# Optimization experiments

Measured on AMD Instinct MI355X. Metric: run time of the kernel, lower is better.

The kernel has to match this reference:

```python
import jax, jax.numpy as jnp
import numpy as np

N = 10000
E = 160000
D = 512
EDGE_DIM = 128
L = 3
LN_EPS = 1e-5


def setup_inputs() -> dict:
    key = jax.random.key(0)
    ks = jax.random.split(key, 16)
    s = 0.02
    return {
        "x": jax.random.normal(ks[0], (N, D), dtype=jnp.float32),
        "edge_index": jax.random.randint(ks[1], (2, E), 0, N, dtype=jnp.int64),
        "edge_attr": jax.random.normal(ks[2], (E, EDGE_DIM), dtype=jnp.float32),
        # per-layer GINEConv edge projection Linear(edge_dim -> d_in); here d_in == D for all layers
        "We": jax.random.normal(ks[3], (L, EDGE_DIM, D), dtype=jnp.float32) * s,
        "be": jnp.zeros((L, D), dtype=jnp.float32),
        "eps": jnp.zeros((L,), dtype=jnp.float32),  # train_eps=True, init 0
        # per-layer MLP: Linear(D->D), ReLU, Linear(D->D)
        "W1": jax.random.normal(ks[4], (L, D, D), dtype=jnp.float32) * s,
        "b1": jnp.zeros((L, D), dtype=jnp.float32),
        "W2": jax.random.normal(ks[5], (L, D, D), dtype=jnp.float32) * s,
        "b2": jnp.zeros((L, D), dtype=jnp.float32),
        # per-layer LayerNorm
        "gamma": jnp.ones((L, D), dtype=jnp.float32),
        "beta": jnp.zeros((L, D), dtype=jnp.float32),
        # final Linear(D->D)
        "Wf": jax.random.normal(ks[6], (D, D), dtype=jnp.float32) * s,
        "bf": jnp.zeros((D,), dtype=jnp.float32),
    }


def reference(x, edge_index, edge_attr, We, be, eps, W1, b1, W2, b2, gamma, beta, Wf, bf):
    src = edge_index[0]  # x_j (source)
    dst = edge_index[1]  # aggregation target i
    n = x.shape[0]
    h = x
    for l in range(L):
        # GINEConv message: relu(x_j + lin(edge_attr)), scatter-add at dst
        e = jax.nn.relu(h[src] + edge_attr @ We[l] + be[l])  # [E, D]
        agg = jax.ops.segment_sum(e, dst, num_segments=n)     # [N, D]
        g = (1.0 + eps[l]) * h + agg
        # 2-layer MLP
        g = jax.nn.relu(g @ W1[l] + b1[l]) @ W2[l] + b2[l]
        # ReLU then LayerNorm (dropout p=0)
        g = jax.nn.relu(g)
        mu = jnp.mean(g, axis=-1, keepdims=True)
        var = jnp.mean(jnp.square(g - mu), axis=-1, keepdims=True)
        h = (g - mu) * jax.lax.rsqrt(var + LN_EPS) * gamma[l] + beta[l]
    return h @ Wf + bf
```

## Files before the change

### kernel.cpp

```cpp
#include <hip/hip_runtime.h>

#define NN 10000
#define EE 160000
#define DD 512
#define EDIM 128
#define LLAYERS 3
#define LN_EPS 1e-5f

typedef __attribute__((ext_vector_type(8))) short bf16x8;
typedef __attribute__((ext_vector_type(4))) float f32x4;

__device__ __forceinline__ unsigned short f2b(float f) {
    union { float f; unsigned u; } v; v.f = f;
    unsigned r = (v.u + 0x7fffu + ((v.u >> 16) & 1u)) >> 16;
    return (unsigned short)r;
}
__device__ __forceinline__ float b2f(unsigned short s) {
    union { unsigned u; float f; } v; v.u = ((unsigned)s) << 16;
    return v.f;
}
__device__ __forceinline__ unsigned short f2h(float f) {
    _Float16 h = (_Float16)f;
    unsigned short u; __builtin_memcpy(&u, &h, 2);
    return u;
}
__device__ __forceinline__ float h2f(unsigned short u) {
    _Float16 h; __builtin_memcpy(&h, &u, 2);
    return (float)h;
}

__global__ __launch_bounds__(256) void hist_kernel(
    const int* __restrict__ dstv, int* __restrict__ deg)
{
    int e = blockIdx.x * 256 + threadIdx.x;
    if (e < EE) atomicAdd(&deg[dstv[e]], 1);
}

__global__ __launch_bounds__(256) void scan_kernel(
    const int* __restrict__ deg, int* __restrict__ base, int* __restrict__ cursor)
{
    __shared__ int sums[256];
    const int t = threadIdx.x;
    const int CH = 40;
    int lo = t * CH;
    int hi = lo + CH; if (hi > NN) hi = NN;
    int s = 0;
    for (int i = lo; i < hi; i++) s += deg[i];
    sums[t] = s;
    __syncthreads();
    for (int off = 1; off < 256; off <<= 1) {
        int v = (t >= off) ? sums[t - off] : 0;
        __syncthreads();
        sums[t] += v;
        __syncthreads();
    }
    int run = (t == 0) ? 0 : sums[t - 1];
    for (int i = lo; i < hi; i++) {
        base[i] = run; cursor[i] = run;
        run += deg[i];
    }
}

__global__ __launch_bounds__(256) void scatter_kernel(
    const int* __restrict__ srcv, const int* __restrict__ dstv,
    int* __restrict__ cursor,
    int* __restrict__ ssrc, int* __restrict__ sdst, int* __restrict__ perm)
{
    int e = blockIdx.x * 256 + threadIdx.x;
    if (e < EE) {
        int d = dstv[e];
        int pos = atomicAdd(&cursor[d], 1);
        ssrc[pos] = srcv[e];
        sdst[pos] = d;
        perm[pos] = e;
    }
}

__global__ __launch_bounds__(256) void transpose_bf16_kernel(
    const float* __restrict__ src, unsigned short* __restrict__ dst, int K, int N)
{
    __shared__ float t[32][33];
    const int x = threadIdx.x & 31;
    const int y = threadIdx.x >> 5;
    const int bn = blockIdx.x * 32;
    const int bk = blockIdx.y * 32;
    #pragma unroll
    for (int j = 0; j < 32; j += 8)
        t[y + j][x] = src[(size_t)(bk + y + j) * N + bn + x];
    __syncthreads();
    #pragma unroll
    for (int j = 0; j < 32; j += 8)
        dst[(size_t)(bn + y + j) * K + bk + x] = f2b(t[x][y + j]);
}

__global__ __launch_bounds__(256) void cvt_bf16_kernel(
    const float* __restrict__ src, unsigned short* __restrict__ dst)
{
    int i = blockIdx.x * 256 + threadIdx.x;
    float4 v = ((const float4*)src)[i];
    uint2 o;
    o.x = (unsigned)f2b(v.x) | ((unsigned)f2b(v.y) << 16);
    o.y = (unsigned)f2b(v.z) | ((unsigned)f2b(v.w) << 16);
    ((uint2*)dst)[i] = o;
}

__global__ __launch_bounds__(256) void gather_cvt_kernel(
    const float* __restrict__ ea, const int* __restrict__ perm,
    unsigned short* __restrict__ out, int elo)
{
    int i = blockIdx.x * 256 + threadIdx.x;
    int r = i >> 5, c4 = (i & 31) * 4;
    const float* p = ea + (size_t)perm[elo + r] * EDIM + c4;
    float4 v = *(const float4*)p;
    uint2 o;
    o.x = (unsigned)f2b(v.x) | ((unsigned)f2b(v.y) << 16);
    o.y = (unsigned)f2b(v.z) | ((unsigned)f2b(v.w) << 16);
    *(uint2*)&out[(size_t)r * EDIM + c4] = o;
}

#define MEP 136
__global__ __launch_bounds__(256) void msg_gemm(
    const unsigned short* __restrict__ Abf,
    const unsigned short* __restrict__ WeT,
    const float* __restrict__ be,
    unsigned short* __restrict__ msg)
{
    __shared__ unsigned short sA[128 * MEP];

    const int tid  = threadIdx.x;
    const int c0   = blockIdx.x * 128;
    const int e0   = blockIdx.y * 128;
    const int w    = tid >> 6;
    const int lane = tid & 63;
    const int quad = lane >> 4;
    const int l16  = lane & 15;
    const int mh   = (w & 1) * 64;
    const int nsl  = (w >> 1) * 64;

    for (int i = tid; i < 128 * 16; i += 256) {
        int r = i >> 4, seg = i & 15;
        *(uint4*)&sA[r * MEP + seg * 8] =
            *(const uint4*)&Abf[(size_t)(e0 + r) * EDIM + seg * 8];
    }
    __syncthreads();

    f32x4 acc[4][4];
    #pragma unroll
    for (int mr = 0; mr < 4; mr++)
        #pragma unroll
        for (int nb = 0; nb < 4; nb++)
            acc[mr][nb] = (f32x4){0.f, 0.f, 0.f, 0.f};

    #pragma unroll
    for (int ks = 0; ks < 4; ks++) {
        const int ko = ks * 32 + quad * 8;
        bf16x8 a[4];
        #pragma unroll
        for (int mr = 0; mr < 4; mr++)
            a[mr] = *(const bf16x8*)&sA[(mh + mr * 16 + l16) * MEP + ko];
        bf16x8 b[4];
        #pragma unroll
        for (int nb = 0; nb < 4; nb++)
            b[nb] = *(const bf16x8*)&WeT[(size_t)(c0 + nsl + nb * 16 + l16) * EDIM + ko];
        #pragma unroll
        for (int mr = 0; mr < 4; mr++)
            #pragma unroll
            for (int nb = 0; nb < 4; nb++)
                acc[mr][nb] = __builtin_amdgcn_mfma_f32_16x16x32_bf16(a[mr], b[nb], acc[mr][nb], 0, 0, 0);
    }

    #pragma unroll
    for (int mr = 0; mr < 4; mr++) {
        const int rb = e0 + mh + mr * 16 + quad * 4;
        #pragma unroll
        for (int nb = 0; nb < 4; nb++) {
            const int c = c0 + nsl + nb * 16 + l16;
            const float bv = be[c];
            const f32x4 v = acc[mr][nb];
            #pragma unroll
            for (int reg = 0; reg < 4; reg++)
                msg[(size_t)(rb + reg) * DD + c] = f2h(v[reg] + bv);
        }
    }
}

__global__ __launch_bounds__(256) void agg_kernel(
    const unsigned short* __restrict__ h_bf,
    const unsigned short* __restrict__ msg,
    const int* __restrict__ ssrc,
    const int* __restrict__ basep,
    const int* __restrict__ degp,
    const float* __restrict__ epsp,
    float* __restrict__ aggp,
    unsigned short* __restrict__ aprime,
    int elo, int ehi, int first, int last)
{
    const int d  = blockIdx.x;
    const int b0 = basep[d];
    const int b1 = b0 + degp[d];
    int lo = b0 > elo ? b0 : elo;
    int hi = b1 < ehi ? b1 : ehi;
    if (!first && !last && lo >= hi) return;

    const int t  = threadIdx.x;
    const int c2 = t * 2;

    float a0 = 0.f, a1 = 0.f;
    if (!first) {
        float2 pv = *(const float2*)&aggp[(size_t)d * DD + c2];
        a0 = pv.x; a1 = pv.y;
    }
    for (int p = lo; p < hi; p++) {
        const int s = ssrc[p];
        unsigned mv = *(const unsigned*)&msg[(size_t)(p - elo) * DD + c2];
        unsigned hv = *(const unsigned*)&h_bf[(size_t)s * DD + c2];
        a0 += fmaxf(h2f((unsigned short)(mv & 0xffffu)) + b2f((unsigned short)(hv & 0xffffu)), 0.f);
        a1 += fmaxf(h2f((unsigned short)(mv >> 16))     + b2f((unsigned short)(hv >> 16)),     0.f);
    }
    if (last) {
        const float es = 1.0f + epsp[0];
        unsigned hv = *(const unsigned*)&h_bf[(size_t)d * DD + c2];
        unsigned o = (unsigned)f2b(es * b2f((unsigned short)(hv & 0xffffu)) + a0)
                   | ((unsigned)f2b(es * b2f((unsigned short)(hv >> 16))    + a1) << 16);
        *(unsigned*)&aprime[(size_t)d * DD + c2] = o;
    } else {
        *(float2*)&aggp[(size_t)d * DD + c2] = make_float2(a0, a1);
    }
}

#define GPITCH 136
template <bool RELU, bool OUTBF>
__global__ __launch_bounds__(256) void mfma_gemm(
    const unsigned short* __restrict__ A,
    const unsigned short* __restrict__ WT,
    const float* __restrict__ bias,
    void* __restrict__ Cout, int M)
{
    __shared__ unsigned short sA[64 * GPITCH];
    __shared__ unsigned short sB[128 * GPITCH];

    const int tid  = threadIdx.x;
    const int m0   = blockIdx.x * 64;
    const int c0   = blockIdx.y * 128;
    const int w    = tid >> 6;
    const int lane = tid & 63;
    const int quad = lane >> 4;
    const int l16  = lane & 15;
    const int mh   = (w & 1) * 32;
    const int nsl  = (w >> 1) * 64;

    f32x4 acc[2][4];
    #pragma unroll
    for (int mr = 0; mr < 2; mr++)
        #pragma unroll
        for (int nb = 0; nb < 4; nb++)
            acc[mr][nb] = (f32x4){0.f, 0.f, 0.f, 0.f};

    for (int kc = 0; kc < DD; kc += 128) {
        __syncthreads();
        for (int i = tid; i < 64 * 16; i += 256) {
            int r = i >> 4, seg = i & 15;
            int gm = m0 + r;
            uint4 v = make_uint4(0u, 0u, 0u, 0u);
            if (gm < M)
                v = *(const uint4*)&A[(size_t)gm * DD + kc + seg * 8];
            *(uint4*)&sA[r * GPITCH + seg * 8] = v;
        }
        for (int i = tid; i < 128 * 16; i += 256) {
            int r = i >> 4, seg = i & 15;
            *(uint4*)&sB[r * GPITCH + seg * 8] =
                *(const uint4*)&WT[(size_t)(c0 + r) * DD + kc + seg * 8];
        }
        __syncthreads();
        #pragma unroll
        for (int ks = 0; ks < 4; ks++) {
            const int ko = ks * 32 + quad * 8;
            bf16x8 a0 = *(const bf16x8*)&sA[(mh + l16) * GPITCH + ko];
            bf16x8 a1 = *(const bf16x8*)&sA[(mh + 16 + l16) * GPITCH + ko];
            bf16x8 b[4];
            #pragma unroll
            for (int nb = 0; nb < 4; nb++)
                b[nb] = *(const bf16x8*)&sB[(nsl + nb * 16 + l16) * GPITCH + ko];
            #pragma unroll
            for (int nb = 0; nb < 4; nb++) {
                acc[0][nb] = __builtin_amdgcn_mfma_f32_16x16x32_bf16(a0, b[nb], acc[0][nb], 0, 0, 0);
                acc[1][nb] = __builtin_amdgcn_mfma_f32_16x16x32_bf16(a1, b[nb], acc[1][nb], 0, 0, 0);
            }
        }
    }

    #pragma unroll
    for (int mr = 0; mr < 2; mr++) {
        const int rbase = m0 + mh + mr * 16 + quad * 4;
        #pragma unroll
        for (int nb = 0; nb < 4; nb++) {
            const int c = c0 + nsl + nb * 16 + l16;
            const float bv = bias[c];
            const f32x4 v = acc[mr][nb];
            #pragma unroll
            for (int reg = 0; reg < 4; reg++) {
                int gm = rbase + reg;
                if (gm < M) {
                    float val = v[reg] + bv;
                    if (RELU) val = fmaxf(val, 0.f);
                    if (OUTBF) ((unsigned short*)Cout)[(size_t)gm * DD + c] = f2b(val);
                    else       ((float*)Cout)[(size_t)gm * DD + c] = val;
                }
            }
        }
    }
}

__global__ __launch_bounds__(256) void relu_ln_kernel(
    const unsigned short* __restrict__ g2,
    const float* __restrict__ gamma,
    const float* __restrict__ beta,
    unsigned short* __restrict__ hout)
{
    __shared__ float ss[4], ssq[4];
    const int row = blockIdx.x;
    const int tid = threadIdx.x;
    const unsigned short* gr = g2 + (size_t)row * DD;

    float v0 = fmaxf(b2f(gr[tid]), 0.f);
    float v1 = fmaxf(b2f(gr[tid + 256]), 0.f);
    float s  = v0 + v1;
    float sq = v0 * v0 + v1 * v1;
    #pragma unroll
    for (int off = 32; off > 0; off >>= 1) {
        s  += __shfl_down(s, off);
        sq += __shfl_down(sq, off);
    }
    const int wave = tid >> 6;
    const int lane = tid & 63;
    if (lane == 0) { ss[wave] = s; ssq[wave] = sq; }
    __syncthreads();
    if (tid == 0) {
        float S  = ss[0] + ss[1] + ss[2] + ss[3];
        float SQ = ssq[0] + ssq[1] + ssq[2] + ssq[3];
        float mu = S * (1.f / 512.f);
        float var = SQ * (1.f / 512.f) - mu * mu;
        ss[0]  = mu;
        ssq[0] = rsqrtf(var + LN_EPS);
    }
    __syncthreads();
    float mu = ss[0], rstd = ssq[0];
    hout[(size_t)row * DD + tid] =
        f2b((v0 - mu) * rstd * gamma[tid] + beta[tid]);
    hout[(size_t)row * DD + tid + 256] =
        f2b((v1 - mu) * rstd * gamma[tid + 256] + beta[tid + 256]);
}

extern "C" void kernel_launch(void* const* d_in, const int* in_sizes, int n_in,
                              void* d_out, int out_size, void* d_ws, size_t ws_size,
                              hipStream_t stream)
{
    (void)in_sizes; (void)n_in; (void)out_size;

    const float* x          = (const float*)d_in[0];
    const int*   edge_index = (const int*)d_in[1];
    const float* edge_attr  = (const float*)d_in[2];
    const float* We         = (const float*)d_in[3];
    const float* be         = (const float*)d_in[4];
    const float* eps        = (const float*)d_in[5];
    const float* W1         = (const float*)d_in[6];
    const float* b1         = (const float*)d_in[7];
    const float* W2         = (const float*)d_in[8];
    const float* b2         = (const float*)d_in[9];
    const float* gamma      = (const float*)d_in[10];
    const float* beta       = (const float*)d_in[11];
    const float* Wf         = (const float*)d_in[12];
    const float* bf         = (const float*)d_in[13];

    unsigned short* h_bf   = (unsigned short*)d_ws;
    unsigned short* aprime = h_bf + (size_t)NN * DD;
    unsigned short* t1     = aprime + (size_t)NN * DD;
    unsigned short* t2     = t1 + (size_t)NN * DD;
    unsigned short* WeT    = t2 + (size_t)NN * DD;
    unsigned short* W1T    = WeT + (size_t)LLAYERS * DD * EDIM;
    unsigned short* W2T    = W1T + (size_t)LLAYERS * DD * DD;
    unsigned short* WfT    = W2T + (size_t)LLAYERS * DD * DD;
    int* deg    = (int*)(WfT + (size_t)DD * DD);
    int* basep  = deg + NN;
    int* cursor = basep + NN;
    int* ssrc   = cursor + NN;
    int* sdst   = ssrc + EE;
    int* perm   = sdst + EE;
    float* aggp = (float*)(perm + EE);
    unsigned short* ea_hf = (unsigned short*)(aggp + (size_t)NN * DD);

    size_t used = (size_t)((unsigned char*)ea_hf - (unsigned char*)d_ws);
    size_t rem  = ws_size > used ? ws_size - used : 0;
    const size_t EA_FULL  = (size_t)EE * EDIM * 2;
    const size_t MSG_FULL = (size_t)EE * DD * 2;
    int ea_full; long long capE;
    if (rem >= EA_FULL + MSG_FULL) {
        ea_full = 1; capE = EE;
    } else if (rem >= EA_FULL + (size_t)32 * 1024 * 1024) {
        ea_full = 1;
        capE = (long long)((rem - EA_FULL) / ((size_t)DD * 2)) & ~127LL;
    } else {
        ea_full = 0;
        capE = (long long)(rem / ((size_t)(EDIM + DD) * 2)) & ~127LL;
        if (capE < 128) capE = 128;
    }
    if (capE > EE) capE = EE;
    unsigned short* msg = ea_hf + (ea_full ? (size_t)EE * EDIM : (size_t)capE * EDIM);

    const int* srcv = edge_index;
    const int* dstv = edge_index + EE;

    hipMemsetAsync(deg, 0, NN * sizeof(int), stream);
    hist_kernel<<<dim3((EE + 255) / 256), 256, 0, stream>>>(dstv, deg);
    scan_kernel<<<dim3(1), 256, 0, stream>>>(deg, basep, cursor);
    scatter_kernel<<<dim3((EE + 255) / 256), 256, 0, stream>>>(
        srcv, dstv, cursor, ssrc, sdst, perm);

    cvt_bf16_kernel<<<dim3(NN * DD / 4 / 256), 256, 0, stream>>>(x, h_bf);
    for (int l = 0; l < LLAYERS; l++) {
        transpose_bf16_kernel<<<dim3(DD / 32, EDIM / 32), 256, 0, stream>>>(
            We + (size_t)l * EDIM * DD, WeT + (size_t)l * DD * EDIM, EDIM, DD);
        transpose_bf16_kernel<<<dim3(DD / 32, DD / 32), 256, 0, stream>>>(
            W1 + (size_t)l * DD * DD, W1T + (size_t)l * DD * DD, DD, DD);
        transpose_bf16_kernel<<<dim3(DD / 32, DD / 32), 256, 0, stream>>>(
            W2 + (size_t)l * DD * DD, W2T + (size_t)l * DD * DD, DD, DD);
    }
    transpose_bf16_kernel<<<dim3(DD / 32, DD / 32), 256, 0, stream>>>(Wf, WfT, DD, DD);

    if (ea_full)
        gather_cvt_kernel<<<dim3(EE / 8), 256, 0, stream>>>(edge_attr, perm, ea_hf, 0);

    dim3 ggrid((NN + 63) / 64, DD / 128);

    const int nch = (int)((EE + capE - 1) / capE);
    for (int l = 0; l < LLAYERS; l++) {
        for (int c = 0; c < nch; c++) {
            const int elo = (int)((long long)c * capE);
            const int cnt = (EE - elo < capE) ? (EE - elo) : (int)capE;
            if (!ea_full)
                gather_cvt_kernel<<<dim3(cnt / 8), 256, 0, stream>>>(edge_attr, perm, ea_hf, elo);
            const unsigned short* Ab = ea_full ? ea_hf + (size_t)elo * EDIM : ea_hf;
            msg_gemm<<<dim3(4, cnt / 128), 256, 0, stream>>>(
                Ab, WeT + (size_t)l * DD * EDIM, be + (size_t)l * DD, msg);
            agg_kernel<<<dim3(NN), 256, 0, stream>>>(
                h_bf, msg, ssrc, basep, deg, eps + l, aggp, aprime,
                elo, elo + cnt, c == 0 ? 1 : 0, c == nch - 1 ? 1 : 0);
        }
        mfma_gemm<true, true><<<ggrid, 256, 0, stream>>>(
            aprime, W1T + (size_t)l * DD * DD, b1 + (size_t)l * DD, t1, NN);
        mfma_gemm<false, true><<<ggrid, 256, 0, stream>>>(
            t1, W2T + (size_t)l * DD * DD, b2 + (size_t)l * DD, t2, NN);
        relu_ln_kernel<<<dim3(NN), 256, 0, stream>>>(
            t2, gamma + (size_t)l * DD, beta + (size_t)l * DD, h_bf);
    }
    mfma_gemm<false, false><<<ggrid, 256, 0, stream>>>(h_bf, WfT, bf, d_out, NN);
}
```

Before: 834.6 us.

## Unify GEMMs into 128x128 tile kernel with LDS-staged coalesced stores, unroll aggregation

Replaces the separate message GEMM and the 64x128 MLP GEMM with one templated 128x128-tile kernel. It reads B fragments straight from global memory instead of staging them in LDS, and writes 16-bit outputs through LDS so the global stores are coalesced and wide. Message stores are nontemporal. The aggregation loop is unrolled by four and its message reads use nontemporal loads, so more independent loads are in flight. This raises per-block work and register use, gives fewer blocks for the N-sized GEMMs, and makes B reads uncached in LDS.

```diff
diff --git a/kernel.cpp b/kernel.cpp
--- a/kernel.cpp
+++ b/kernel.cpp
@@ -9,6 +9,7 @@
 
 typedef __attribute__((ext_vector_type(8))) short bf16x8;
 typedef __attribute__((ext_vector_type(4))) float f32x4;
+typedef __attribute__((ext_vector_type(4))) unsigned int u32x4;
 
 __device__ __forceinline__ unsigned short f2b(float f) {
     union { float f; unsigned u; } v; v.f = f;
@@ -119,17 +120,18 @@
 }
 
 #define MEP 136
-__global__ __launch_bounds__(256) void msg_gemm(
-    const unsigned short* __restrict__ Abf,
-    const unsigned short* __restrict__ WeT,
-    const float* __restrict__ be,
-    unsigned short* __restrict__ msg)
+template <int KDIM, bool RELU, int OUT>
+__global__ __launch_bounds__(256) void tile_gemm(
+    const unsigned short* __restrict__ A,
+    const unsigned short* __restrict__ WT,
+    const float* __restrict__ bias,
+    void* __restrict__ Cout, int M)
 {
     __shared__ unsigned short sA[128 * MEP];
 
     const int tid  = threadIdx.x;
     const int c0   = blockIdx.x * 128;
-    const int e0   = blockIdx.y * 128;
+    const int m0   = blockIdx.y * 128;
     const int w    = tid >> 6;
     const int lane = tid & 63;
     const int quad = lane >> 4;
@@ -137,13 +139,6 @@
     const int mh   = (w & 1) * 64;
     const int nsl  = (w >> 1) * 64;
 
-    for (int i = tid; i < 128 * 16; i += 256) {
-        int r = i >> 4, seg = i & 15;
-        *(uint4*)&sA[r * MEP + seg * 8] =
-            *(const uint4*)&Abf[(size_t)(e0 + r) * EDIM + seg * 8];
-    }
-    __syncthreads();
-
     f32x4 acc[4][4];
     #pragma unroll
     for (int mr = 0; mr < 4; mr++)
@@ -151,35 +146,87 @@
         for (int nb = 0; nb < 4; nb++)
             acc[mr][nb] = (f32x4){0.f, 0.f, 0.f, 0.f};
 
-    #pragma unroll
-    for (int ks = 0; ks < 4; ks++) {
-        const int ko = ks * 32 + quad * 8;
-        bf16x8 a[4];
+    for (int kc = 0; kc < KDIM; kc += 128) {
+        if (kc) __syncthreads();
+        for (int i = tid; i < 128 * 16; i += 256) {
+            int r = i >> 4, seg = i & 15;
+            int gm = m0 + r;
+            u32x4 v = (u32x4){0u, 0u, 0u, 0u};
+            if (gm < M)
+                v = *(const u32x4*)&A[(size_t)gm * KDIM + kc + seg * 8];
+            *(u32x4*)&sA[r * MEP + seg * 8] = v;
+        }
+        __syncthreads();
         #pragma unroll
-        for (int mr = 0; mr < 4; mr++)
-            a[mr] = *(const bf16x8*)&sA[(mh + mr * 16 + l16) * MEP + ko];
-        bf16x8 b[4];
-        #pragma unroll
-        for (int nb = 0; nb < 4; nb++)
-            b[nb] = *(const bf16x8*)&WeT[(size_t)(c0 + nsl + nb * 16 + l16) * EDIM + ko];
-        #pragma unroll
-        for (int mr = 0; mr < 4; mr++)
+        for (int ks = 0; ks < 4; ks++) {
+            const int ko = ks * 32 + quad * 8;
+            bf16x8 a[4];
+            #pragma unroll
+            for (int mr = 0; mr < 4; mr++)
+                a[mr] = *(const bf16x8*)&sA[(mh + mr * 16 + l16) * MEP + ko];
+            bf16x8 b[4];
             #pragma unroll
             for (int nb = 0; nb < 4; nb++)
-                acc[mr][nb] = __builtin_amdgcn_mfma_f32_16x16x32_bf16(a[mr], b[nb], acc[mr][nb], 0, 0, 0);
-    }
-
-    #pragma unroll
-    for (int mr = 0; mr < 4; mr++) {
-        const int rb = e0 + mh + mr * 16 + quad * 4;
+                b[nb] = *(const bf16x8*)&WT[(size_t)(c0 + nsl + nb * 16 + l16) * KDIM + kc + ko];
+            #pragma unroll
+            for (int mr = 0; mr < 4; mr++)
+                #pragma unroll
+                for (int nb = 0; nb < 4; nb++)
+                    acc[mr][nb] = __builtin_amdgcn_mfma_f32_16x16x32_bf16(a[mr], b[nb], acc[mr][nb], 0, 0, 0);
+        }
+    }
+
+    if (OUT == 2) {
+        float* Co = (float*)Cout;
         #pragma unroll
-        for (int nb = 0; nb < 4; nb++) {
-            const int c = c0 + nsl + nb * 16 + l16;
-            const float bv = be[c];
-            const f32x4 v = acc[mr][nb];
+        for (int mr = 0; mr < 4; mr++) {
+            const int rb = m0 + mh + mr * 16 + quad * 4;
             #pragma unroll
-            for (int reg = 0; reg < 4; reg++)
-                msg[(size_t)(rb + reg) * DD + c] = f2h(v[reg] + bv);
+            for (int nb = 0; nb < 4; nb++) {
+                const int c = c0 + nsl + nb * 16 + l16;
+                const float bv = bias[c];
+                const f32x4 v = acc[mr][nb];
+                #pragma unroll
+                for (int reg = 0; reg < 4; reg++) {
+                    int gm = rb + reg;
+                    if (gm < M) {
+                        float val = v[reg] + bv;
+                        if (RELU) val = fmaxf(val, 0.f);
+                        Co[(size_t)gm * DD + c] = val;
+                    }
+                }
+            }
+        }
+    } else {
+        __syncthreads();
+        #pragma unroll
+        for (int mr = 0; mr < 4; mr++) {
+            const int lr = mh + mr * 16 + quad * 4;
+            #pragma unroll
+            for (int nb = 0; nb < 4; nb++) {
+                const int lc = nsl + nb * 16 + l16;
+                const float bv = bias[c0 + lc];
+                const f32x4 v = acc[mr][nb];
+                #pragma unroll
+                for (int reg = 0; reg < 4; reg++) {
+                    float val = v[reg] + bv;
+                    if (RELU) val = fmaxf(val, 0.f);
+                    sA[(lr + reg) * MEP + lc] = (OUT == 0) ? f2b(val) : f2h(val);
+                }
+            }
+        }
+        __syncthreads();
+        unsigned short* Co = (unsigned short*)Cout;
+        for (int i = tid; i < 128 * 16; i += 256) {
+            int r = i >> 4, seg = i & 15;
+            int gm = m0 + r;
+            if (gm < M) {
+                u32x4 v = *(const u32x4*)&sA[r * MEP + seg * 8];
+                if (OUT == 1)
+                    __builtin_nontemporal_store(v, (u32x4*)&Co[(size_t)gm * DD + c0 + seg * 8]);
+                else
+                    *(u32x4*)&Co[(size_t)gm * DD + c0 + seg * 8] = v;
+            }
         }
     }
 }
@@ -210,9 +257,30 @@
         float2 pv = *(const float2*)&aggp[(size_t)d * DD + c2];
         a0 = pv.x; a1 = pv.y;
     }
-    for (int p = lo; p < hi; p++) {
+    int p = lo;
+    for (; p + 4 <= hi; p += 4) {
+        const int s0 = ssrc[p],     s1 = ssrc[p + 1];
+        const int s2 = ssrc[p + 2], s3 = ssrc[p + 3];
+        unsigned m0v = __builtin_nontemporal_load((const unsigned*)&msg[(size_t)(p     - elo) * DD + c2]);
+        unsigned m1v = __builtin_nontemporal_load((const unsigned*)&msg[(size_t)(p + 1 - elo) * DD + c2]);
+        unsigned m2v = __builtin_nontemporal_load((const unsigned*)&msg[(size_t)(p + 2 - elo) * DD + c2]);
+        unsigned m3v = __builtin_nontemporal_load((const unsigned*)&msg[(size_t)(p + 3 - elo) * DD + c2]);
+        unsigned h0v = *(const unsigned*)&h_bf[(size_t)s0 * DD + c2];
+        unsigned h1v = *(const unsigned*)&h_bf[(size_t)s1 * DD + c2];
+        unsigned h2v = *(const unsigned*)&h_bf[(size_t)s2 * DD + c2];
+        unsigned h3v = *(const unsigned*)&h_bf[(size_t)s3 * DD + c2];
+        a0 += fmaxf(h2f((unsigned short)(m0v & 0xffffu)) + b2f((unsigned short)(h0v & 0xffffu)), 0.f);
+        a1 += fmaxf(h2f((unsigned short)(m0v >> 16))     + b2f((unsigned short)(h0v >> 16)),     0.f);
+        a0 += fmaxf(h2f((unsigned short)(m1v & 0xffffu)) + b2f((unsigned short)(h1v & 0xffffu)), 0.f);
+        a1 += fmaxf(h2f((unsigned short)(m1v >> 16))     + b2f((unsigned short)(h1v >> 16)),     0.f);
+        a0 += fmaxf(h2f((unsigned short)(m2v & 0xffffu)) + b2f((unsigned short)(h2v & 0xffffu)), 0.f);
+        a1 += fmaxf(h2f((unsigned short)(m2v >> 16))     + b2f((unsigned short)(h2v >> 16)),     0.f);
+        a0 += fmaxf(h2f((unsigned short)(m3v & 0xffffu)) + b2f((unsigned short)(h3v & 0xffffu)), 0.f);
+        a1 += fmaxf(h2f((unsigned short)(m3v >> 16))     + b2f((unsigned short)(h3v >> 16)),     0.f);
+    }
+    for (; p < hi; p++) {
         const int s = ssrc[p];
-        unsigned mv = *(const unsigned*)&msg[(size_t)(p - elo) * DD + c2];
+        unsigned mv = __builtin_nontemporal_load((const unsigned*)&msg[(size_t)(p - elo) * DD + c2]);
         unsigned hv = *(const unsigned*)&h_bf[(size_t)s * DD + c2];
         a0 += fmaxf(h2f((unsigned short)(mv & 0xffffu)) + b2f((unsigned short)(hv & 0xffffu)), 0.f);
         a1 += fmaxf(h2f((unsigned short)(mv >> 16))     + b2f((unsigned short)(hv >> 16)),     0.f);
@@ -225,89 +293,6 @@
         *(unsigned*)&aprime[(size_t)d * DD + c2] = o;
     } else {
         *(float2*)&aggp[(size_t)d * DD + c2] = make_float2(a0, a1);
-    }
-}
-
-#define GPITCH 136
-template <bool RELU, bool OUTBF>
-__global__ __launch_bounds__(256) void mfma_gemm(
-    const unsigned short* __restrict__ A,
-    const unsigned short* __restrict__ WT,
-    const float* __restrict__ bias,
-    void* __restrict__ Cout, int M)
-{
-    __shared__ unsigned short sA[64 * GPITCH];
-    __shared__ unsigned short sB[128 * GPITCH];
-
-    const int tid  = threadIdx.x;
-    const int m0   = blockIdx.x * 64;
-    const int c0   = blockIdx.y * 128;
-    const int w    = tid >> 6;
-    const int lane = tid & 63;
-    const int quad = lane >> 4;
-    const int l16  = lane & 15;
-    const int mh   = (w & 1) * 32;
-    const int nsl  = (w >> 1) * 64;
-
-    f32x4 acc[2][4];
-    #pragma unroll
-    for (int mr = 0; mr < 2; mr++)
-        #pragma unroll
-        for (int nb = 0; nb < 4; nb++)
-            acc[mr][nb] = (f32x4){0.f, 0.f, 0.f, 0.f};
-
-    for (int kc = 0; kc < DD; kc += 128) {
-        __syncthreads();
-        for (int i = tid; i < 64 * 16; i += 256) {
-            int r = i >> 4, seg = i & 15;
-            int gm = m0 + r;
-            uint4 v = make_uint4(0u, 0u, 0u, 0u);
-            if (gm < M)
-                v = *(const uint4*)&A[(size_t)gm * DD + kc + seg * 8];
-            *(uint4*)&sA[r * GPITCH + seg * 8] = v;
-        }
-        for (int i = tid; i < 128 * 16; i += 256) {
-            int r = i >> 4, seg = i & 15;
-            *(uint4*)&sB[r * GPITCH + seg * 8] =
-                *(const uint4*)&WT[(size_t)(c0 + r) * DD + kc + seg * 8];
-        }
-        __syncthreads();
-        #pragma unroll
-        for (int ks = 0; ks < 4; ks++) {
-            const int ko = ks * 32 + quad * 8;
-            bf16x8 a0 = *(const bf16x8*)&sA[(mh + l16) * GPITCH + ko];
-            bf16x8 a1 = *(const bf16x8*)&sA[(mh + 16 + l16) * GPITCH + ko];
-            bf16x8 b[4];
-            #pragma unroll
-            for (int nb = 0; nb < 4; nb++)
-                b[nb] = *(const bf16x8*)&sB[(nsl + nb * 16 + l16) * GPITCH + ko];
-            #pragma unroll
-            for (int nb = 0; nb < 4; nb++) {
-                acc[0][nb] = __builtin_amdgcn_mfma_f32_16x16x32_bf16(a0, b[nb], acc[0][nb], 0, 0, 0);
-                acc[1][nb] = __builtin_amdgcn_mfma_f32_16x16x32_bf16(a1, b[nb], acc[1][nb], 0, 0, 0);
-            }
-        }
-    }
-
-    #pragma unroll
-    for (int mr = 0; mr < 2; mr++) {
-        const int rbase = m0 + mh + mr * 16 + quad * 4;
-        #pragma unroll
-        for (int nb = 0; nb < 4; nb++) {
-            const int c = c0 + nsl + nb * 16 + l16;
-            const float bv = bias[c];
-            const f32x4 v = acc[mr][nb];
-            #pragma unroll
-            for (int reg = 0; reg < 4; reg++) {
-                int gm = rbase + reg;
-                if (gm < M) {
-                    float val = v[reg] + bv;
-                    if (RELU) val = fmaxf(val, 0.f);
-                    if (OUTBF) ((unsigned short*)Cout)[(size_t)gm * DD + c] = f2b(val);
-                    else       ((float*)Cout)[(size_t)gm * DD + c] = val;
-                }
-            }
-        }
     }
 }
 
@@ -430,7 +415,7 @@
     if (ea_full)
         gather_cvt_kernel<<<dim3(EE / 8), 256, 0, stream>>>(edge_attr, perm, ea_hf, 0);
 
-    dim3 ggrid((NN + 63) / 64, DD / 128);
+    dim3 ggrid(DD / 128, (NN + 127) / 128);
 
     const int nch = (int)((EE + capE - 1) / capE);
     for (int l = 0; l < LLAYERS; l++) {
@@ -440,18 +425,18 @@
             if (!ea_full)
                 gather_cvt_kernel<<<dim3(cnt / 8), 256, 0, stream>>>(edge_attr, perm, ea_hf, elo);
             const unsigned short* Ab = ea_full ? ea_hf + (size_t)elo * EDIM : ea_hf;
-            msg_gemm<<<dim3(4, cnt / 128), 256, 0, stream>>>(
-                Ab, WeT + (size_t)l * DD * EDIM, be + (size_t)l * DD, msg);
+            tile_gemm<EDIM, false, 1><<<dim3(4, cnt / 128), 256, 0, stream>>>(
+                Ab, WeT + (size_t)l * DD * EDIM, be + (size_t)l * DD, msg, cnt);
             agg_kernel<<<dim3(NN), 256, 0, stream>>>(
                 h_bf, msg, ssrc, basep, deg, eps + l, aggp, aprime,
                 elo, elo + cnt, c == 0 ? 1 : 0, c == nch - 1 ? 1 : 0);
         }
-        mfma_gemm<true, true><<<ggrid, 256, 0, stream>>>(
+        tile_gemm<DD, true, 0><<<ggrid, 256, 0, stream>>>(
             aprime, W1T + (size_t)l * DD * DD, b1 + (size_t)l * DD, t1, NN);
-        mfma_gemm<false, true><<<ggrid, 256, 0, stream>>>(
+        tile_gemm<DD, false, 0><<<ggrid, 256, 0, stream>>>(
             t1, W2T + (size_t)l * DD * DD, b2 + (size_t)l * DD, t2, NN);
         relu_ln_kernel<<<dim3(NN), 256, 0, stream>>>(
             t2, gamma + (size_t)l * DD, beta + (size_t)l * DD, h_bf);
     }
-    mfma_gemm<false, false><<<ggrid, 256, 0, stream>>>(h_bf, WfT, bf, d_out, NN);
-}
+    tile_gemm<DD, false, 2><<<ggrid, 256, 0, stream>>>(h_bf, WfT, bf, d_out, NN);
+}
```

Measured after the change: 874.3 us. +4.8%, slower.
